# Kernel optimization log

Hardware: AMD Instinct MI355X
Metric: run time of the kernel (lower is better)

The kernel has to match this reference:

```python
import jax, jax.numpy as jnp
import numpy as np
import math

DIM = 4096
N_HEADS = 32
HEAD_DIM = DIM // N_HEADS  # 128
SEQLEN = 2048


def setup_inputs() -> dict:
    key = jax.random.key(0)
    ks = jax.random.split(key, 8)
    x = jax.random.normal(ks[0], (1, SEQLEN, DIM), dtype=jnp.float32)
    # freqs_cis as real view: (seqlen, head_dim//2, 2) = (cos, sin) of rotary angles
    theta = 10000.0 ** (-jnp.arange(0, HEAD_DIM, 2, dtype=jnp.float32) / HEAD_DIM)
    angles = jnp.arange(SEQLEN, dtype=jnp.float32)[:, None] * theta[None, :]
    freqs = jnp.stack([jnp.cos(angles), jnp.sin(angles)], axis=-1)  # (S, 64, 2)
    # causal additive mask (use -1e9 instead of -inf for numeric safety)
    mask = jnp.triu(jnp.full((SEQLEN, SEQLEN), -1e9, dtype=jnp.float32), k=1)[None, None]
    scale = 1.0 / math.sqrt(DIM)
    wq = jax.random.normal(ks[1], (DIM, DIM), dtype=jnp.float32) * scale
    wk = jax.random.normal(ks[2], (DIM, DIM), dtype=jnp.float32) * scale
    wv = jax.random.normal(ks[3], (DIM, DIM), dtype=jnp.float32) * scale
    wo = jax.random.normal(ks[4], (DIM, DIM), dtype=jnp.float32) * scale
    return {"x": x, "start_pos": 0, "freqs": freqs, "mask": mask,
            "wq": wq, "wk": wk, "wv": wv, "wo": wo}


def _rotary(xq, xk, freqs, seqlen, n_heads, head_dim):
    # Faithful to source: note the repo's slice(0, 2) means xq_ == xq (no pair swap).
    ll = freqs[:, :, 0:1]  # (S, hd/2, 1) cos
    rr = freqs[:, :, 1:2]  # (S, hd/2, 1) sin
    fl = jnp.concatenate([ll, ll], axis=-1).reshape(seqlen, 1, head_dim)
    fr = jnp.concatenate([-rr, rr], axis=-1).reshape(seqlen, 1, head_dim)
    xq_ = xq.reshape(seqlen, n_heads, head_dim // 2, 2).reshape(seqlen, n_heads, head_dim)  # == xq
    xk_ = xk.reshape(seqlen, n_heads, head_dim // 2, 2).reshape(seqlen, n_heads, head_dim)  # == xk
    return xq * fl + xq_ * fr, xk * fl + xk_ * fr


def reference(x, start_pos, freqs, mask, wq, wk, wv, wo):
    bsz, seqlen, dim = x.shape  # bsz == 1 (source squeezes batch)
    xs = x[0]  # (S, D) -- HE encrypt/linear/decrypt roundtrip == plain linear
    xq = xs @ wq.T
    xk = xs @ wk.T
    xv = xs @ wv.T
    xq = xq.reshape(seqlen, N_HEADS, HEAD_DIM)
    xk = xk.reshape(seqlen, N_HEADS, HEAD_DIM)
    xv = xv.reshape(seqlen, N_HEADS, HEAD_DIM)
    xq, xk = _rotary(xq, xk, freqs, seqlen, N_HEADS, HEAD_DIM)
    # start_pos == 0 and zero-initialized cache => keys/values are just xk/xv
    q = jnp.transpose(xq, (1, 0, 2))  # (H, S, Dh)
    k = jnp.transpose(xk, (1, 0, 2))
    v = jnp.transpose(xv, (1, 0, 2))
    scores = jnp.einsum('hqd,hkd->hqk', q, k) / math.sqrt(HEAD_DIM)  # (H, S, S)
    scores = scores[None] + mask  # (1, H, S, S)
    probs = jax.nn.softmax(scores, axis=-1)
    out = jnp.einsum('bhqk,hkd->bhqd', probs, v)  # (1, H, S, Dh)
    out = jnp.transpose(out, (0, 2, 1, 3)).reshape(bsz, seqlen, dim)
    return out @ wo.T
```

## Files before the change

kernel.cpp:

```cpp
#include <hip/hip_runtime.h>

#define DIM 4096
#define SEQ 2048
#define NH 32
#define HD 128

typedef __bf16 bf16x8 __attribute__((ext_vector_type(8)));
typedef float f32x4 __attribute__((ext_vector_type(4)));

#define QSCALE 0.12751649736765598f

__device__ inline ushort f2bf(float f) {
    union { float f; unsigned u; } v; v.f = f;
    unsigned r = v.u + 0x7fffu + ((v.u >> 16) & 1u);
    return (ushort)(r >> 16);
}

__global__ void conv_all(const float* __restrict__ x,  const float* __restrict__ wq,
                         const float* __restrict__ wk, const float* __restrict__ wv,
                         const float* __restrict__ wo,
                         ushort* __restrict__ xb,  ushort* __restrict__ wqb,
                         ushort* __restrict__ wkb, ushort* __restrict__ wvb,
                         ushort* __restrict__ wob) {
    int i = blockIdx.x * 256 + threadIdx.x;
    const float* src; ushort* dst; int off;
    const int n4x = (SEQ * DIM) / 4;
    if (i < n4x) { src = x; dst = xb; off = i; }
    else {
        int j = i - n4x;
        int w = j >> 22;
        off = j & ((1 << 22) - 1);
        src = (w == 0) ? wq : (w == 1) ? wk : (w == 2) ? wv : wo;
        dst = (w == 0) ? wqb : (w == 1) ? wkb : (w == 2) ? wvb : wob;
    }
    float4 v = ((const float4*)src)[off];
    ushort4 o;
    o.x = f2bf(v.x); o.y = f2bf(v.y); o.z = f2bf(v.z); o.w = f2bf(v.w);
    ((ushort4*)dst)[off] = o;
}


#define AS1(p) (const __attribute__((address_space(1))) void*)(p)
#define AS3(p) (__attribute__((address_space(3))) void*)(p)
#define FENCE() asm volatile("" ::: "memory")
#define BARRIER() do { FENCE(); __builtin_amdgcn_s_barrier(); FENCE(); } while (0)

__device__ __forceinline__ void gemm256_body(
    const ushort* __restrict__ Ab,
    const ushort* __restrict__ Bb,
    ushort* __restrict__ sA0, ushort* __restrict__ sA1,
    ushort* __restrict__ sB0, ushort* __restrict__ sB1,
    f32x4 acc[8][4], const int K)
{
    const int tid  = threadIdx.x;
    const int wave = tid >> 6, lane = tid & 63;
    const int quad = lane >> 4, c = lane & 15;
    const int wm = wave >> 2, wn = wave & 3;

    const int aoff  = (lane >> 3) * K + (((lane & 7) ^ (lane >> 3)) * 8);
    const int sa_r0 = wave * 8;
    const int sb_r0 = (wave >> 1) * 64 + (wave & 1) * 16;

    const int rp0 = (quad ^ (c & 7)) * 8;
    const int rp1 = ((4 + quad) ^ (c & 7)) * 8;
    const int arow = (wm * 128 + c) * 64;
    const int brow = (wn * 64 + c) * 64;

#define STAGE_A(dst, h, k0) do { \
    const int _r0 = (h) * 64 + sa_r0; \
    __builtin_amdgcn_global_load_lds(AS1(Ab + (size_t)_r0 * K + (k0) + aoff), \
                                     AS3((dst) + _r0 * 64), 16, 0, 0); \
    const int _r1 = _r0 + 128; \
    __builtin_amdgcn_global_load_lds(AS1(Ab + (size_t)_r1 * K + (k0) + aoff), \
                                     AS3((dst) + _r1 * 64), 16, 0, 0); \
  } while (0)
#define STAGE_B(dst, h, k0) do { \
    const int _r0 = (h) * 32 + sb_r0; \
    __builtin_amdgcn_global_load_lds(AS1(Bb + (size_t)_r0 * K + (k0) + aoff), \
                                     AS3((dst) + _r0 * 64), 16, 0, 0); \
    const int _r1 = _r0 + 8; \
    __builtin_amdgcn_global_load_lds(AS1(Bb + (size_t)_r1 * K + (k0) + aoff), \
                                     AS3((dst) + _r1 * 64), 16, 0, 0); \
  } while (0)

    bf16x8 af[4][2], bfr[4][2];

#define READ_A(buf, mh) do { \
    _Pragma("unroll") \
    for (int _m = 0; _m < 4; ++_m) { \
        af[_m][0] = *(const bf16x8*)&(buf)[arow + (mh) * 4096 + _m * 1024 + rp0]; \
        af[_m][1] = *(const bf16x8*)&(buf)[arow + (mh) * 4096 + _m * 1024 + rp1]; \
    } } while (0)
#define READ_B2(buf, nh) do { \
    _Pragma("unroll") \
    for (int _n = 0; _n < 2; ++_n) { \
        bfr[(nh) * 2 + _n][0] = *(const bf16x8*)&(buf)[brow + (nh) * 2048 + _n * 1024 + rp0]; \
        bfr[(nh) * 2 + _n][1] = *(const bf16x8*)&(buf)[brow + (nh) * 2048 + _n * 1024 + rp1]; \
    } } while (0)
#define MMA_Q(mh, nq) do { \
    __builtin_amdgcn_s_setprio(1); \
    _Pragma("unroll") \
    for (int _kk = 0; _kk < 2; ++_kk) \
    _Pragma("unroll") \
    for (int _m = 0; _m < 4; ++_m) \
    _Pragma("unroll") \
    for (int _n = 0; _n < 2; ++_n) \
        acc[(mh) * 4 + _m][(nq) * 2 + _n] = __builtin_amdgcn_mfma_f32_16x16x32_bf16( \
            af[_m][_kk], bfr[(nq) * 2 + _n][_kk], acc[(mh) * 4 + _m][(nq) * 2 + _n], 0, 0, 0); \
    __builtin_amdgcn_s_setprio(0); \
  } while (0)

    const int NT = K >> 6;

    STAGE_A(sA0, 0, 0);  STAGE_A(sA0, 1, 0);
    STAGE_B(sB0, 0, 0);  STAGE_B(sB0, 1, 0);
    STAGE_A(sA1, 0, 64); STAGE_A(sA1, 1, 64);
    STAGE_B(sB1, 0, 64); STAGE_B(sB1, 1, 64);
    asm volatile("s_waitcnt vmcnt(8)" ::: "memory");
    BARRIER();

#pragma unroll 1
    for (int t = 0; t < NT; ++t) {
        ushort* cA = (t & 1) ? sA1 : sA0;
        ushort* cB = (t & 1) ? sB1 : sB0;
        const int kn2 = (t + 2) << 6;
        const bool ok2 = (t + 2 < NT);

        READ_A(cA, 0); READ_B2(cB, 0);
        BARRIER();
        MMA_Q(0, 0);
        BARRIER();

        READ_B2(cB, 1);
        if (ok2) { STAGE_A(cA, 0, kn2); STAGE_B(cB, 0, kn2); }
        BARRIER();
        MMA_Q(0, 1);
        BARRIER();

        READ_A(cA, 1);
        if (ok2) STAGE_B(cB, 1, kn2);
        BARRIER();
        MMA_Q(1, 0);
        BARRIER();

        if (ok2) STAGE_A(cA, 1, kn2);
        BARRIER();
        MMA_Q(1, 1);
        if (t < NT - 1) {
            if (ok2) asm volatile("s_waitcnt vmcnt(8)" ::: "memory");
            else     asm volatile("s_waitcnt vmcnt(0)" ::: "memory");
        }
        BARRIER();
    }
#undef STAGE_A
#undef STAGE_B
#undef READ_A
#undef READ_B2
#undef MMA_Q
}

__global__ __launch_bounds__(512, 2)
void gemm_qkv(const ushort* __restrict__ A,
              const ushort* __restrict__ Bq, const ushort* __restrict__ Bk,
              const ushort* __restrict__ Bv,
              ushort* __restrict__ qout, ushort* __restrict__ kout,
              ushort* __restrict__ vt, const float* __restrict__ freqs) {
    __shared__ __align__(16) ushort sA[2][256 * 64];
    __shared__ __align__(16) ushort sB[2][256 * 64];
    const int bi = blockIdx.x;
    const int x = bi & 7;
    const int l = bi >> 3;
    const int mblk = l & 7;
    const int nblk = x * 6 + (l >> 3);
    const int wsel = nblk >> 4;
    const int nloc = (nblk & 15) * 256;
    const int m0 = mblk * 256;
    const ushort* B = (wsel == 0) ? Bq : (wsel == 1) ? Bk : Bv;

    const f32x4 vzero = {0.f, 0.f, 0.f, 0.f};
    f32x4 acc[8][4];
#pragma unroll
    for (int i = 0; i < 8; i++)
#pragma unroll
        for (int j = 0; j < 4; j++) acc[i][j] = vzero;

    gemm256_body(A + (size_t)m0 * DIM, B + (size_t)nloc * DIM,
                 &sA[0][0], &sA[1][0], &sB[0][0], &sB[1][0], acc, DIM);

    const int tid = threadIdx.x;
    const int wave = tid >> 6, lane = tid & 63;
    const int quad = lane >> 4, c = lane & 15;
    const int wm = wave >> 2, wn = wave & 3;

    if (wsel < 2) {
        ushort* Cw = wsel ? kout : qout;
        const float qs = wsel ? 1.0f : QSCALE;
#pragma unroll
        for (int i = 0; i < 8; i++) {
#pragma unroll
            for (int j = 0; j < 4; j++) {
                int colg = nloc + wn * 64 + j * 16 + c;
                int dh = (colg & 127) >> 1;
#pragma unroll
                for (int r = 0; r < 4; r++) {
                    int row = m0 + wm * 128 + i * 16 + quad * 4 + r;
                    float2 f2 = ((const float2*)freqs)[row * 64 + dh];
                    float f = (f2.x + ((c & 1) ? f2.y : -f2.y)) * qs;
                    Cw[(size_t)row * DIM + colg] = f2bf(acc[i][j][r] * f);
                }
            }
        }
    } else {
#pragma unroll
        for (int i = 0; i < 8; i++) {
#pragma unroll
            for (int j = 0; j < 4; j++) {
                int cv = nloc + wn * 64 + j * 16 + c;
                int row0 = m0 + wm * 128 + i * 16 + quad * 4;
                ushort4 o;
                o.x = f2bf(acc[i][j][0]); o.y = f2bf(acc[i][j][1]);
                o.z = f2bf(acc[i][j][2]); o.w = f2bf(acc[i][j][3]);
                *(ushort4*)&vt[(size_t)cv * SEQ + row0] = o;
            }
        }
    }
}

__global__ __launch_bounds__(512, 2)
void gemm_f32out(const ushort* __restrict__ A, const ushort* __restrict__ B,
                 float* __restrict__ C, int M, int N, int K) {
    __shared__ __align__(16) ushort sA[2][256 * 64];
    __shared__ __align__(16) ushort sB[2][256 * 64];
    const int bi = blockIdx.x;
    const int x = bi & 7;
    const int l = bi >> 3;
    const int mblk = l & 7;
    const int nblk = x * 2 + (l >> 3);
    const int m0 = mblk * 256, n0 = nblk * 256;

    const f32x4 vzero = {0.f, 0.f, 0.f, 0.f};
    f32x4 acc[8][4];
#pragma unroll
    for (int i = 0; i < 8; i++)
#pragma unroll
        for (int j = 0; j < 4; j++) acc[i][j] = vzero;

    gemm256_body(A + (size_t)m0 * K, B + (size_t)n0 * K,
                 &sA[0][0], &sA[1][0], &sB[0][0], &sB[1][0], acc, K);

    const int tid = threadIdx.x;
    const int wave = tid >> 6, lane = tid & 63;
    const int quad = lane >> 4, c = lane & 15;
    const int wm = wave >> 2, wn = wave & 3;

#pragma unroll
    for (int i = 0; i < 8; i++)
#pragma unroll
        for (int j = 0; j < 4; j++)
#pragma unroll
            for (int r = 0; r < 4; r++) {
                int row = m0 + wm * 128 + i * 16 + quad * 4 + r;
                int col = n0 + wn * 64 + j * 16 + c;
                C[(size_t)row * N + col] = acc[i][j][r];
            }
}

__global__ __launch_bounds__(256)
void flash_kernel(const ushort* __restrict__ Q, const ushort* __restrict__ K,
                  const ushort* __restrict__ Vt, ushort* __restrict__ O) {
    const int bi = blockIdx.x;
    const int h = bi & (NH - 1);
    const int p = bi >> 5;
    __shared__ __align__(16) ushort sK[2][64 * 128];
    __shared__ __align__(16) ushort sVt[2][128 * 64];
    __shared__ __align__(16) ushort sP[4][16 * 72];
    const int tid = threadIdx.x, wave = tid >> 6, lane = tid & 63;
    const int quad = lane >> 4, c = lane & 15;

#define STAGE_KV(db, kt) do { \
    _Pragma("unroll") \
    for (int _i = 0; _i < 4; _i++) { \
        int _lr = wave * 16 + _i * 4 + (lane >> 4); \
        int _ch = lane & 15; \
        int _g = (_ch & 8) | ((_ch ^ _lr) & 7); \
        __builtin_amdgcn_global_load_lds( \
            AS1(K + (size_t)((kt) * 64 + _lr) * DIM + h * HD + _g * 8), \
            AS3(&sK[db][(wave * 16 + _i * 4) * 128]), 16, 0, 0); \
    } \
    _Pragma("unroll") \
    for (int _i = 0; _i < 4; _i++) { \
        int _ld = wave * 32 + _i * 8 + (lane >> 3); \
        int _ch = lane & 7; \
        int _g = (_ch ^ _ld) & 7; \
        __builtin_amdgcn_global_load_lds( \
            AS1(Vt + (size_t)(h * HD + _ld) * SEQ + (kt) * 64 + _g * 8), \
            AS3(&sVt[db][(wave * 32 + _i * 8) * 64]), 16, 0, 0); \
    } } while (0)

    for (int pass = 0; pass < 2; pass++) {
        const int qb = pass ? (SEQ / 64 - 1 - p) : p;
        const int q0 = qb * 64;

        bf16x8 qf[4];
        {
            const ushort* Qp = Q + (size_t)(q0 + wave * 16 + c) * DIM + h * HD;
#pragma unroll
            for (int ks = 0; ks < 4; ks++) qf[ks] = *(const bf16x8*)(Qp + ks * 32 + quad * 8);
        }
        const f32x4 vzero = {0.f, 0.f, 0.f, 0.f};
        f32x4 oa[8];
#pragma unroll
        for (int dt = 0; dt < 8; dt++) oa[dt] = vzero;
        float ms[4], ls[4];
#pragma unroll
        for (int r = 0; r < 4; r++) { ms[r] = -1e30f; ls[r] = 0.f; }

        STAGE_KV(0, 0);

#pragma unroll 1
        for (int kt = 0; kt <= qb; kt++) {
            const int b = kt & 1;
            if (kt < qb) {
                STAGE_KV(b ^ 1, kt + 1);
                asm volatile("s_waitcnt vmcnt(8)" ::: "memory");
            } else {
                asm volatile("s_waitcnt vmcnt(0)" ::: "memory");
            }
            BARRIER();

            f32x4 s[4];
#pragma unroll
            for (int nt = 0; nt < 4; nt++) s[nt] = vzero;
            __builtin_amdgcn_s_setprio(1);
#pragma unroll
            for (int ks = 0; ks < 4; ks++)
#pragma unroll
                for (int nt = 0; nt < 4; nt++) {
                    int lr = nt * 16 + c;
                    int gc = ks * 4 + quad;
                    int pch = (gc & 8) | ((gc ^ lr) & 7);
                    bf16x8 kf = *(const bf16x8*)&sK[b][lr * 128 + pch * 8];
                    s[nt] = __builtin_amdgcn_mfma_f32_16x16x32_bf16(qf[ks], kf, s[nt], 0, 0, 0);
                }
            __builtin_amdgcn_s_setprio(0);

            if (kt == qb) {
#pragma unroll
                for (int nt = 0; nt < 4; nt++)
#pragma unroll
                    for (int r = 0; r < 4; r++) {
                        int keyg = nt * 16 + c;
                        int qg   = wave * 16 + quad * 4 + r;
                        if (keyg > qg) s[nt][r] = -1e30f;
                    }
            }

            float mnew[4], alpha[4];
#pragma unroll
            for (int r = 0; r < 4; r++) {
                float v = fmaxf(fmaxf(s[0][r], s[1][r]), fmaxf(s[2][r], s[3][r]));
                v = fmaxf(v, __shfl_xor(v, 1));
                v = fmaxf(v, __shfl_xor(v, 2));
                v = fmaxf(v, __shfl_xor(v, 4));
                v = fmaxf(v, __shfl_xor(v, 8));
                mnew[r]  = fmaxf(ms[r], v);
                alpha[r] = exp2f(ms[r] - mnew[r]);
                ms[r]    = mnew[r];
            }
            float rs[4] = {0.f, 0.f, 0.f, 0.f};
#pragma unroll
            for (int nt = 0; nt < 4; nt++)
#pragma unroll
                for (int r = 0; r < 4; r++) {
                    float pv = exp2f(s[nt][r] - mnew[r]);
                    rs[r] += pv;
                    sP[wave][(quad * 4 + r) * 72 + nt * 16 + c] = f2bf(pv);
                }
#pragma unroll
            for (int r = 0; r < 4; r++) {
                float v = rs[r];
                v += __shfl_xor(v, 1);
                v += __shfl_xor(v, 2);
                v += __shfl_xor(v, 4);
                v += __shfl_xor(v, 8);
                ls[r] = ls[r] * alpha[r] + v;
            }
#pragma unroll
            for (int dt = 0; dt < 8; dt++)
#pragma unroll
                for (int r = 0; r < 4; r++) oa[dt][r] *= alpha[r];

            __asm__ volatile("s_waitcnt lgkmcnt(0)" ::: "memory");

            __builtin_amdgcn_s_setprio(1);
#pragma unroll
            for (int k2 = 0; k2 < 2; k2++) {
                bf16x8 pf = *(const bf16x8*)&sP[wave][c * 72 + k2 * 32 + quad * 8];
#pragma unroll
                for (int dt = 0; dt < 8; dt++) {
                    int ld = dt * 16 + c;
                    int gc = k2 * 4 + quad;
                    int pch = (gc ^ ld) & 7;
                    bf16x8 vf = *(const bf16x8*)&sVt[b][ld * 64 + pch * 8];
                    oa[dt] = __builtin_amdgcn_mfma_f32_16x16x32_bf16(pf, vf, oa[dt], 0, 0, 0);
                }
            }
            __builtin_amdgcn_s_setprio(0);

            BARRIER();
        }

#pragma unroll
        for (int r = 0; r < 4; r++) {
            float inv = 1.f / ls[r];
            int row = q0 + wave * 16 + quad * 4 + r;
#pragma unroll
            for (int dt = 0; dt < 8; dt++)
                O[(size_t)row * DIM + h * HD + dt * 16 + c] = f2bf(oa[dt][r] * inv);
        }
    }
#undef STAGE_KV
}

extern "C" void kernel_launch(void* const* d_in, const int* in_sizes, int n_in,
                              void* d_out, int out_size, void* d_ws, size_t ws_size,
                              hipStream_t stream) {
    const float* x     = (const float*)d_in[0];
    const float* freqs = (const float*)d_in[2];
    const float* wq    = (const float*)d_in[4];
    const float* wk    = (const float*)d_in[5];
    const float* wv    = (const float*)d_in[6];
    const float* wo    = (const float*)d_in[7];
    float* out = (float*)d_out;

    ushort* xb    = (ushort*)d_ws;
    ushort* wqb   = xb    + (size_t)SEQ * DIM;
    ushort* wkb   = wqb   + (size_t)DIM * DIM;
    ushort* wvb   = wkb   + (size_t)DIM * DIM;
    ushort* wob   = wvb   + (size_t)DIM * DIM;
    ushort* qbuf  = wob   + (size_t)DIM * DIM;
    ushort* kbuf  = qbuf  + (size_t)SEQ * DIM;
    ushort* vtbuf = kbuf  + (size_t)SEQ * DIM;
    ushort* obuf  = vtbuf + (size_t)SEQ * DIM;

    const int n4tot = (SEQ * DIM + 4 * DIM * DIM) / 4;
    conv_all<<<n4tot / 256, 256, 0, stream>>>(x, wq, wk, wv, wo, xb, wqb, wkb, wvb, wob);

    gemm_qkv<<<dim3(384), 512, 0, stream>>>(xb, wqb, wkb, wvb, qbuf, kbuf, vtbuf, freqs);

    flash_kernel<<<dim3(NH * SEQ / 128), 256, 0, stream>>>(qbuf, kbuf, vtbuf, obuf);

    gemm_f32out<<<dim3(128), 512, 0, stream>>>(obuf, wob, out, SEQ, DIM, DIM);
}
```

Baseline: 757.2 us.

## Split-K the output projection and reorder GEMM main-loop B fragment prefetch

The output projection GEMM is split into two K halves, so 256 blocks run instead of 128 and the GPU's CUs are filled better. The second half writes partials into the reused wq bf16 workspace, and a new add_partial kernel sums them into the output. The shared GEMM body also reorders its loop: it preloads the first B fragment half before the loop and stages the next tile's B earlier, so LDS reads overlap with the MFMA work. The cost is an extra fp32 round-trip of 32 MB through memory plus one more kernel launch.

```diff
diff --git a/kernel.cpp b/kernel.cpp
--- a/kernel.cpp
+++ b/kernel.cpp
@@ -50,14 +50,14 @@
     const ushort* __restrict__ Bb,
     ushort* __restrict__ sA0, ushort* __restrict__ sA1,
     ushort* __restrict__ sB0, ushort* __restrict__ sB1,
-    f32x4 acc[8][4], const int K)
+    f32x4 acc[8][4], const int ldk, const int klen)
 {
     const int tid  = threadIdx.x;
     const int wave = tid >> 6, lane = tid & 63;
     const int quad = lane >> 4, c = lane & 15;
     const int wm = wave >> 2, wn = wave & 3;
 
-    const int aoff  = (lane >> 3) * K + (((lane & 7) ^ (lane >> 3)) * 8);
+    const int aoff  = (lane >> 3) * ldk + (((lane & 7) ^ (lane >> 3)) * 8);
     const int sa_r0 = wave * 8;
     const int sb_r0 = (wave >> 1) * 64 + (wave & 1) * 16;
 
@@ -68,36 +68,38 @@
 
 #define STAGE_A(dst, h, k0) do { \
     const int _r0 = (h) * 64 + sa_r0; \
-    __builtin_amdgcn_global_load_lds(AS1(Ab + (size_t)_r0 * K + (k0) + aoff), \
+    __builtin_amdgcn_global_load_lds(AS1(Ab + (size_t)_r0 * ldk + (k0) + aoff), \
                                      AS3((dst) + _r0 * 64), 16, 0, 0); \
     const int _r1 = _r0 + 128; \
-    __builtin_amdgcn_global_load_lds(AS1(Ab + (size_t)_r1 * K + (k0) + aoff), \
+    __builtin_amdgcn_global_load_lds(AS1(Ab + (size_t)_r1 * ldk + (k0) + aoff), \
                                      AS3((dst) + _r1 * 64), 16, 0, 0); \
   } while (0)
 #define STAGE_B(dst, h, k0) do { \
     const int _r0 = (h) * 32 + sb_r0; \
-    __builtin_amdgcn_global_load_lds(AS1(Bb + (size_t)_r0 * K + (k0) + aoff), \
+    __builtin_amdgcn_global_load_lds(AS1(Bb + (size_t)_r0 * ldk + (k0) + aoff), \
                                      AS3((dst) + _r0 * 64), 16, 0, 0); \
     const int _r1 = _r0 + 8; \
-    __builtin_amdgcn_global_load_lds(AS1(Bb + (size_t)_r1 * K + (k0) + aoff), \
+    __builtin_amdgcn_global_load_lds(AS1(Bb + (size_t)_r1 * ldk + (k0) + aoff), \
                                      AS3((dst) + _r1 * 64), 16, 0, 0); \
   } while (0)
 
-    bf16x8 af[4][2], bfr[4][2];
-
-#define READ_A(buf, mh) do { \
+    bf16x8 af[4][2];
+    bf16x8 b0[2][2];
+    bf16x8 b1[2][2];
+
+#define READ_AH(buf, mh) do { \
     _Pragma("unroll") \
     for (int _m = 0; _m < 4; ++_m) { \
         af[_m][0] = *(const bf16x8*)&(buf)[arow + (mh) * 4096 + _m * 1024 + rp0]; \
         af[_m][1] = *(const bf16x8*)&(buf)[arow + (mh) * 4096 + _m * 1024 + rp1]; \
     } } while (0)
-#define READ_B2(buf, nh) do { \
+#define READ_BH(buf, nh, dst) do { \
     _Pragma("unroll") \
     for (int _n = 0; _n < 2; ++_n) { \
-        bfr[(nh) * 2 + _n][0] = *(const bf16x8*)&(buf)[brow + (nh) * 2048 + _n * 1024 + rp0]; \
-        bfr[(nh) * 2 + _n][1] = *(const bf16x8*)&(buf)[brow + (nh) * 2048 + _n * 1024 + rp1]; \
+        dst[_n][0] = *(const bf16x8*)&(buf)[brow + (nh) * 2048 + _n * 1024 + rp0]; \
+        dst[_n][1] = *(const bf16x8*)&(buf)[brow + (nh) * 2048 + _n * 1024 + rp1]; \
     } } while (0)
-#define MMA_Q(mh, nq) do { \
+#define MMA_Q(mh, nq, B) do { \
     __builtin_amdgcn_s_setprio(1); \
     _Pragma("unroll") \
     for (int _kk = 0; _kk < 2; ++_kk) \
@@ -106,56 +108,62 @@
     _Pragma("unroll") \
     for (int _n = 0; _n < 2; ++_n) \
         acc[(mh) * 4 + _m][(nq) * 2 + _n] = __builtin_amdgcn_mfma_f32_16x16x32_bf16( \
-            af[_m][_kk], bfr[(nq) * 2 + _n][_kk], acc[(mh) * 4 + _m][(nq) * 2 + _n], 0, 0, 0); \
+            af[_m][_kk], B[_n][_kk], acc[(mh) * 4 + _m][(nq) * 2 + _n], 0, 0, 0); \
     __builtin_amdgcn_s_setprio(0); \
   } while (0)
 
-    const int NT = K >> 6;
-
-    STAGE_A(sA0, 0, 0);  STAGE_A(sA0, 1, 0);
-    STAGE_B(sB0, 0, 0);  STAGE_B(sB0, 1, 0);
-    STAGE_A(sA1, 0, 64); STAGE_A(sA1, 1, 64);
-    STAGE_B(sB1, 0, 64); STAGE_B(sB1, 1, 64);
+    const int NT = klen >> 6;
+
+    STAGE_B(sB0, 0, 0);  STAGE_A(sA0, 0, 0);
+    STAGE_B(sB0, 1, 0);  STAGE_A(sA0, 1, 0);
+    STAGE_B(sB1, 0, 64); STAGE_A(sA1, 0, 64);
+    STAGE_B(sB1, 1, 64); STAGE_A(sA1, 1, 64);
     asm volatile("s_waitcnt vmcnt(8)" ::: "memory");
+    BARRIER();
+    READ_BH(sB0, 0, b0);
     BARRIER();
 
 #pragma unroll 1
     for (int t = 0; t < NT; ++t) {
         ushort* cA = (t & 1) ? sA1 : sA0;
         ushort* cB = (t & 1) ? sB1 : sB0;
+        ushort* nB = (t & 1) ? sB0 : sB1;
         const int kn2 = (t + 2) << 6;
-        const bool ok2 = (t + 2 < NT);
-
-        READ_A(cA, 0); READ_B2(cB, 0);
-        BARRIER();
-        MMA_Q(0, 0);
-        BARRIER();
-
-        READ_B2(cB, 1);
-        if (ok2) { STAGE_A(cA, 0, kn2); STAGE_B(cB, 0, kn2); }
-        BARRIER();
-        MMA_Q(0, 1);
-        BARRIER();
-
-        READ_A(cA, 1);
+        const bool ok1 = (t + 1 < NT), ok2 = (t + 2 < NT);
+
+        READ_AH(cA, 0);
+        if (ok2) STAGE_B(cB, 0, kn2);
+        BARRIER();
+        MMA_Q(0, 0, b0);
+        BARRIER();
+
+        READ_BH(cB, 1, b1);
+        if (ok2) STAGE_A(cA, 0, kn2);
+        BARRIER();
+        MMA_Q(0, 1, b1);
+        BARRIER();
+
+        READ_AH(cA, 1);
         if (ok2) STAGE_B(cB, 1, kn2);
         BARRIER();
-        MMA_Q(1, 0);
-        BARRIER();
-
-        if (ok2) STAGE_A(cA, 1, kn2);
-        BARRIER();
-        MMA_Q(1, 1);
-        if (t < NT - 1) {
-            if (ok2) asm volatile("s_waitcnt vmcnt(8)" ::: "memory");
+        MMA_Q(1, 1, b1);
+        BARRIER();
+
+        if (ok1) {
+            if (ok2) asm volatile("s_waitcnt vmcnt(6)" ::: "memory");
             else     asm volatile("s_waitcnt vmcnt(0)" ::: "memory");
-        }
+            BARRIER();
+            if (ok2) STAGE_A(cA, 1, kn2);
+        }
+        BARRIER();
+        MMA_Q(1, 0, b0);
+        if (ok1) READ_BH(nB, 0, b0);
         BARRIER();
     }
 #undef STAGE_A
 #undef STAGE_B
-#undef READ_A
-#undef READ_B2
+#undef READ_AH
+#undef READ_BH
 #undef MMA_Q
 }
 
@@ -185,7 +193,7 @@
         for (int j = 0; j < 4; j++) acc[i][j] = vzero;
 
     gemm256_body(A + (size_t)m0 * DIM, B + (size_t)nloc * DIM,
-                 &sA[0][0], &sA[1][0], &sB[0][0], &sB[1][0], acc, DIM);
+                 &sA[0][0], &sA[1][0], &sB[0][0], &sB[1][0], acc, DIM, DIM);
 
     const int tid = threadIdx.x;
     const int wave = tid >> 6, lane = tid & 63;
@@ -228,15 +236,19 @@
 
 __global__ __launch_bounds__(512, 2)
 void gemm_f32out(const ushort* __restrict__ A, const ushort* __restrict__ B,
-                 float* __restrict__ C, int M, int N, int K) {
+                 float* __restrict__ C, float* __restrict__ P,
+                 int M, int N, int K) {
     __shared__ __align__(16) ushort sA[2][256 * 64];
     __shared__ __align__(16) ushort sB[2][256 * 64];
     const int bi = blockIdx.x;
-    const int x = bi & 7;
-    const int l = bi >> 3;
+    const int kh = bi >> 7;
+    const int r  = bi & 127;
+    const int x = r & 7;
+    const int l = r >> 3;
     const int mblk = l & 7;
     const int nblk = x * 2 + (l >> 3);
     const int m0 = mblk * 256, n0 = nblk * 256;
+    const int khalf = K >> 1;
 
     const f32x4 vzero = {0.f, 0.f, 0.f, 0.f};
     f32x4 acc[8][4];
@@ -245,24 +257,33 @@
 #pragma unroll
         for (int j = 0; j < 4; j++) acc[i][j] = vzero;
 
-    gemm256_body(A + (size_t)m0 * K, B + (size_t)n0 * K,
-                 &sA[0][0], &sA[1][0], &sB[0][0], &sB[1][0], acc, K);
+    gemm256_body(A + (size_t)m0 * K + kh * khalf, B + (size_t)n0 * K + kh * khalf,
+                 &sA[0][0], &sA[1][0], &sB[0][0], &sB[1][0], acc, K, khalf);
 
     const int tid = threadIdx.x;
     const int wave = tid >> 6, lane = tid & 63;
     const int quad = lane >> 4, c = lane & 15;
     const int wm = wave >> 2, wn = wave & 3;
+    float* dst = kh ? P : C;
 
 #pragma unroll
     for (int i = 0; i < 8; i++)
 #pragma unroll
         for (int j = 0; j < 4; j++)
 #pragma unroll
-            for (int r = 0; r < 4; r++) {
-                int row = m0 + wm * 128 + i * 16 + quad * 4 + r;
+            for (int r2 = 0; r2 < 4; r2++) {
+                int row = m0 + wm * 128 + i * 16 + quad * 4 + r2;
                 int col = n0 + wn * 64 + j * 16 + c;
-                C[(size_t)row * N + col] = acc[i][j][r];
-            }
+                dst[(size_t)row * N + col] = acc[i][j][r2];
+            }
+}
+
+__global__ void add_partial(float* __restrict__ C, const float* __restrict__ P) {
+    int i = blockIdx.x * 256 + threadIdx.x;
+    float4 a = ((const float4*)C)[i];
+    float4 b = ((const float4*)P)[i];
+    a.x += b.x; a.y += b.y; a.z += b.z; a.w += b.w;
+    ((float4*)C)[i] = a;
 }
 
 __global__ __launch_bounds__(256)
@@ -442,6 +463,7 @@
     ushort* kbuf  = qbuf  + (size_t)SEQ * DIM;
     ushort* vtbuf = kbuf  + (size_t)SEQ * DIM;
     ushort* obuf  = vtbuf + (size_t)SEQ * DIM;
+    float* pbuf = (float*)wqb;
 
     const int n4tot = (SEQ * DIM + 4 * DIM * DIM) / 4;
     conv_all<<<n4tot / 256, 256, 0, stream>>>(x, wq, wk, wv, wo, xb, wqb, wkb, wvb, wob);
@@ -450,5 +472,6 @@
 
     flash_kernel<<<dim3(NH * SEQ / 128), 256, 0, stream>>>(qbuf, kbuf, vtbuf, obuf);
 
-    gemm_f32out<<<dim3(128), 512, 0, stream>>>(obuf, wob, out, SEQ, DIM, DIM);
-}
+    gemm_f32out<<<dim3(256), 512, 0, stream>>>(obuf, wob, out, pbuf, SEQ, DIM, DIM);
+    add_partial<<<dim3(SEQ * DIM / 4 / 256), 256, 0, stream>>>(out, pbuf);
+}
```

After: 697.5 us. 7.9% less time.
